# Optimization experiments

Hardware: AMD Instinct MI355X
Metric: run time of the kernel (lower is better)

## Reference

```python
import jax, jax.numpy as jnp
import numpy as np

C = 256      # in/out channels
PSI = 4
W = C // PSI          # window width = 64
D = W // 2            # stride = 32
HEADS = 2 * PSI - 1   # 7


def conv_bn_relu(x, Wmat, scale, bias):
    # 1x1 conv (no bias) + inference-mode BN (folded to per-channel scale/bias) + ReLU
    y = jnp.einsum('oc,bcn->bon', Wmat, x)
    return jax.nn.relu(y * scale[:, None] + bias[:, None])


def setup_inputs() -> dict:
    key = jax.random.key(0)
    ks = jax.random.split(key, 16)
    B, N = 4, 2048
    x = jax.random.normal(ks[0], (B, C, N), dtype=jnp.float32)
    Wq = jax.random.normal(ks[1], (C, C), dtype=jnp.float32) / np.sqrt(C)
    Wk = jax.random.normal(ks[2], (C, C), dtype=jnp.float32) / np.sqrt(C)
    Wv = jax.random.normal(ks[3], (C, C), dtype=jnp.float32) / np.sqrt(C)
    sq = jax.random.uniform(ks[4], (C,), dtype=jnp.float32, minval=0.5, maxval=1.5)
    bq = jax.random.normal(ks[5], (C,), dtype=jnp.float32) * 0.1
    sk = jax.random.uniform(ks[6], (C,), dtype=jnp.float32, minval=0.5, maxval=1.5)
    bk = jax.random.normal(ks[7], (C,), dtype=jnp.float32) * 0.1
    sv = jax.random.uniform(ks[8], (C,), dtype=jnp.float32, minval=0.5, maxval=1.5)
    bv = jax.random.normal(ks[9], (C,), dtype=jnp.float32) * 0.1
    Wf = jax.random.normal(ks[10], (C, HEADS * W), dtype=jnp.float32) / np.sqrt(HEADS * W)
    bf = jax.random.normal(ks[11], (C,), dtype=jnp.float32) * 0.1
    sf = jax.random.uniform(ks[12], (C,), dtype=jnp.float32, minval=0.5, maxval=1.5)
    bff = jax.random.normal(ks[13], (C,), dtype=jnp.float32) * 0.1
    return dict(x=x, Wq=Wq, sq=sq, bq=bq, Wk=Wk, sk=sk, bk=bk,
                Wv=Wv, sv=sv, bv=bv, Wf=Wf, bf=bf, sf=sf, bff=bff)


def reference(x, Wq, sq, bq, Wk, sk, bk, Wv, sv, bv, Wf, bf, sf, bff):
    q = conv_bn_relu(x, Wq, sq, bq)   # [B, C, N]
    k = conv_bn_relu(x, Wk, sk, bk)
    v = conv_bn_relu(x, Wv, sv, bv)

    # overlapping channel windows: head m covers channels [m*D, m*D+W)
    win = jnp.arange(HEADS)[:, None] * D + jnp.arange(W)[None, :]  # [HEADS, W]
    qw = q[:, win, :]  # [B, HEADS, W, N]
    kw = k[:, win, :]
    vw = v[:, win, :]

    # a_m = q_m^T k_m over channel window -> [B, HEADS, N, N]
    attn = jnp.einsum('bhwn,bhwm->bhnm', qw, kw)
    attn = jax.nn.softmax(attn, axis=-1)
    # o_m = (a_m v_m^T)^T -> [B, HEADS, W, N]
    o = jnp.einsum('bhnm,bhwm->bhwn', attn, vw)

    B, _, _, N = o.shape
    O = o.reshape(B, HEADS * W, N)  # concat heads along channel dim

    # fusion: 1x1 conv (with bias) + BN + ReLU
    y = jnp.einsum('oc,bcn->bon', Wf, O) + bf[:, None]
    return jax.nn.relu(y * sf[:, None] + bff[:, None])
```

## Files before the change

kernel.cpp:

```cpp
#include <hip/hip_runtime.h>
#include <hip/hip_bf16.h>

typedef __attribute__((ext_vector_type(8))) short bf16x8;
typedef __attribute__((ext_vector_type(4))) float f32x4;

namespace {
constexpr int kC = 256;
constexpr int kN = 2048;
constexpr int kB = 4;
constexpr int kHeads = 7;
constexpr int kOC = kHeads * 64;
constexpr int kSplit = 2;
constexpr int kMChunk = kN / kSplit;
constexpr float kLog2e = 1.44269504f;
}

static __device__ __forceinline__ float bf2f(ushort u) {
    union { unsigned u; float f; } v; v.u = ((unsigned)u) << 16;
    return v.f;
}
static __device__ __forceinline__ unsigned pk_bf16(float a, float b) {
    __hip_bfloat162 h = __float22bfloat162_rn(make_float2(a, b));
    union { __hip_bfloat162 h; unsigned u; } v; v.h = h;
    return v.u;
}
static __device__ __forceinline__ ushort4 pack4bf(float a, float b, float c, float d) {
    union { ushort4 s; uint2 u; } v;
    v.u.x = pk_bf16(a, b); v.u.y = pk_bf16(c, d);
    return v.s;
}
static __device__ __forceinline__ float fexp2(float x) {
#if __has_builtin(__builtin_amdgcn_exp2f)
    return __builtin_amdgcn_exp2f(x);
#else
    return exp2f(x);
#endif
}
static __device__ __forceinline__ void g2l16(const ushort* g, ushort* l) {
    __builtin_amdgcn_global_load_lds(
        (const __attribute__((address_space(1))) void*)g,
        (__attribute__((address_space(3))) void*)l,
        16, 0, 0);
}

__global__ __launch_bounds__(256) void cast_w_kernel(
    const float* __restrict__ Wq, const float* __restrict__ Wk,
    const float* __restrict__ Wv, const float* __restrict__ Wf,
    ushort* __restrict__ wq, ushort* __restrict__ wk,
    ushort* __restrict__ wv, ushort* __restrict__ wf)
{
    int which = blockIdx.y;
    const float* src = which == 0 ? Wq : which == 1 ? Wk : which == 2 ? Wv : Wf;
    ushort* dst      = which == 0 ? wq : which == 1 ? wk : which == 2 ? wv : wf;
    int n = (which == 3) ? kC * kOC : kC * kC;
    int i = (blockIdx.x * 256 + threadIdx.x) * 4;
    if (i < n) {
        float4 v = *(const float4*)(src + i);
        *(ushort4*)(dst + i) = pack4bf(v.x, v.y, v.z, v.w);
    }
}

__global__ __launch_bounds__(256) void transpose_kernel(
    const float* __restrict__ x, ushort* __restrict__ xT)
{
    const int nt = blockIdx.x, ct = blockIdx.y, b = blockIdx.z;
    __shared__ float T[64][65];
    const int tid = threadIdx.x;
    const float* xb = x + ((size_t)b * kC + ct * 64) * kN + nt * 64;
#pragma unroll
    for (int p = 0; p < 16; ++p) {
        int idx = p * 256 + tid;
        int cc = idx >> 6, nn = idx & 63;
        T[cc][nn] = xb[(size_t)cc * kN + nn];
    }
    __syncthreads();
    ushort* xTb = xT + ((size_t)b * kN + nt * 64) * kC + ct * 64;
#pragma unroll
    for (int p = 0; p < 4; ++p) {
        int nn = p * 16 + (tid >> 4);
        int c4 = (tid & 15) * 4;
        *(ushort4*)&xTb[(size_t)nn * kC + c4] =
            pack4bf(T[c4 + 0][nn], T[c4 + 1][nn], T[c4 + 2][nn], T[c4 + 3][nn]);
    }
}

__global__ __launch_bounds__(256, 2) void qkv_kernel(
    const ushort* __restrict__ xT,
    const ushort* __restrict__ Wqb, const ushort* __restrict__ Wkb, const ushort* __restrict__ Wvb,
    const float* __restrict__ sq, const float* __restrict__ bq,
    const float* __restrict__ sk, const float* __restrict__ bk,
    const float* __restrict__ sv, const float* __restrict__ bv,
    ushort* __restrict__ qT, ushort* __restrict__ kT, ushort* __restrict__ vB)
{
    const int nt  = blockIdx.x;
    const int ot  = blockIdx.y;
    const int b   = blockIdx.z / 3;
    const int mat = blockIdx.z % 3;
    const ushort* Wb = mat == 0 ? Wqb : mat == 1 ? Wkb : Wvb;
    const float* sm = mat == 0 ? sq : mat == 1 ? sk : sv;
    const float* bm = mat == 0 ? bq : mat == 1 ? bk : bv;

    __shared__ __align__(16) ushort lds[4][128 * 64];

    const int tid = threadIdx.x;
    const int lane = tid & 63, wav = tid >> 6;
    const int quad = lane >> 4, l16 = lane & 15;

    const ushort* xTb = xT + ((size_t)b * kN + nt * 128) * kC;
    const ushort* Wt  = Wb + (size_t)(ot * 128) * kC;

    f32x4 acc[8][2];
#pragma unroll
    for (int mt = 0; mt < 8; ++mt)
#pragma unroll
        for (int ntt = 0; ntt < 2; ++ntt)
#pragma unroll
            for (int r = 0; r < 4; ++r) acc[mt][ntt][r] = 0.f;

    const int sa   = lane >> 3;
    const int sblk = (lane & 7) ^ sa;
    auto dmaK = [&](int k0, int buf) {
#pragma unroll
        for (int p = 0; p < 4; ++p) {
            int row = wav * 32 + p * 8 + sa;
            size_t so = (size_t)row * kC + k0 + sblk * 8;
            int dbase = (wav * 32 + p * 8) * 64;
            g2l16(Wt + so,  &lds[buf][dbase]);
            g2l16(xTb + so, &lds[2 + buf][dbase]);
        }
    };

    dmaK(0, 0);
    __syncthreads();

    for (int kt = 0; kt < 4; ++kt) {
        const int cur = kt & 1;
        const bool more = (kt < 3);
        if (more) dmaK((kt + 1) * 64, cur ^ 1);

        const ushort* rowB = (mat < 2) ? lds[cur] : lds[2 + cur];
        const ushort* colB = (mat < 2) ? lds[2 + cur] : lds[cur];
#pragma unroll
        for (int ks = 0; ks < 2; ++ks) {
            bf16x8 bfr[2];
#pragma unroll
            for (int ntt = 0; ntt < 2; ++ntt) {
                int row = wav * 32 + ntt * 16 + l16;
                bfr[ntt] = *(const bf16x8*)&colB[row * 64 + (((ks * 4 + quad) ^ (row & 7)) * 8)];
            }
#pragma unroll
            for (int mt = 0; mt < 8; ++mt) {
                int row = mt * 16 + l16;
                bf16x8 af = *(const bf16x8*)&rowB[row * 64 + (((ks * 4 + quad) ^ (row & 7)) * 8)];
#pragma unroll
                for (int ntt = 0; ntt < 2; ++ntt)
                    acc[mt][ntt] = __builtin_amdgcn_mfma_f32_16x16x32_bf16(
                        af, bfr[ntt], acc[mt][ntt], 0, 0, 0);
            }
        }
        __syncthreads();
    }

    ushort* sT = &lds[0][0];
    const float qs = (mat == 0) ? kLog2e : 1.f;

    if (mat < 2) {
#pragma unroll
        for (int mt = 0; mt < 8; ++mt) {
            float4 sc4 = *(const float4*)&sm[ot * 128 + mt * 16 + quad * 4];
            float4 bi4 = *(const float4*)&bm[ot * 128 + mt * 16 + quad * 4];
#pragma unroll
            for (int ntt = 0; ntt < 2; ++ntt) {
                int nrow = wav * 32 + ntt * 16 + l16;
                float v0 = fmaf(acc[mt][ntt][0], sc4.x, bi4.x) * qs;
                float v1 = fmaf(acc[mt][ntt][1], sc4.y, bi4.y) * qs;
                float v2 = fmaf(acc[mt][ntt][2], sc4.z, bi4.z) * qs;
                float v3 = fmaf(acc[mt][ntt][3], sc4.w, bi4.w) * qs;
                int cb = (mt * 2 + (quad >> 1)) ^ (nrow & 15);
                *(ushort4*)&sT[nrow * 128 + cb * 8 + (quad & 1) * 4] =
                    pack4bf(v0 > 0.f ? v0 : 0.f, v1 > 0.f ? v1 : 0.f,
                            v2 > 0.f ? v2 : 0.f, v3 > 0.f ? v3 : 0.f);
            }
        }
        __syncthreads();
        ushort* out = (mat == 0) ? qT : kT;
#pragma unroll
        for (int p = 0; p < 8; ++p) {
            int idx = p * 256 + tid;
            int row = idx >> 4, blk = idx & 15;
            int4 d = *(const int4*)&sT[row * 128 + ((blk ^ (row & 15)) * 8)];
            *(int4*)&out[((size_t)b * kN + nt * 128 + row) * kC + ot * 128 + blk * 8] = d;
        }
    } else {
#pragma unroll
        for (int ntt = 0; ntt < 2; ++ntt) {
            int orow = wav * 32 + ntt * 16 + l16;
            float sc = sm[ot * 128 + orow], bi = bm[ot * 128 + orow];
#pragma unroll
            for (int mt = 0; mt < 8; ++mt) {
                float v0 = fmaf(acc[mt][ntt][0], sc, bi);
                float v1 = fmaf(acc[mt][ntt][1], sc, bi);
                float v2 = fmaf(acc[mt][ntt][2], sc, bi);
                float v3 = fmaf(acc[mt][ntt][3], sc, bi);
                int cb = (mt * 2 + (quad >> 1)) ^ (orow & 15);
                *(ushort4*)&sT[orow * 128 + cb * 8 + (quad & 1) * 4] =
                    pack4bf(v0 > 0.f ? v0 : 0.f, v1 > 0.f ? v1 : 0.f,
                            v2 > 0.f ? v2 : 0.f, v3 > 0.f ? v3 : 0.f);
            }
        }
        __syncthreads();
#pragma unroll
        for (int p = 0; p < 8; ++p) {
            int idx = p * 256 + tid;
            int row = idx >> 4, blk = idx & 15;
            int4 d = *(const int4*)&sT[row * 128 + ((blk ^ (row & 15)) * 8)];
            *(int4*)&vB[((size_t)b * kC + ot * 128 + row) * kN + nt * 128 + blk * 8] = d;
        }
    }
}

__global__ __launch_bounds__(512, 4) void attn_kernel(
    const ushort* __restrict__ qT, const ushort* __restrict__ kT,
    const ushort* __restrict__ vB,
    ushort* __restrict__ Opart, float* __restrict__ Ls)
{
    const int j   = blockIdx.x;
    const int lid = (j & 7) * 56 + (j >> 3);
    const int nt  = lid & 7;
    const int rest = lid >> 3;
    const int h = rest % 7;
    const int z = rest / 7;
    const int s = z & 1;
    const int b = z >> 1;
    const int n0 = nt * 256;

    const int tid = threadIdx.x;
    const int lane = tid & 63, wav = tid >> 6;
    const int quad = lane >> 4, l16 = lane & 15;

    __shared__ __align__(16) ushort sKV[2][8192];

    const ushort* qTb = qT + (size_t)b * kN * kC;
    const ushort* kTb = kT + (size_t)b * kN * kC;
    const ushort* vbb = vB + ((size_t)b * kC + h * 32) * kN;

    const int arr   = wav >> 2;
    const int rbase = (wav & 3) * 16;

    bf16x8 qf[2][2];
#pragma unroll
    for (int kk = 0; kk < 2; ++kk)
#pragma unroll
        for (int nt2 = 0; nt2 < 2; ++nt2) {
            int ng = n0 + wav * 32 + nt2 * 16 + l16;
            qf[kk][nt2] = *(const bf16x8*)(qTb + (size_t)ng * kC + h * 32 + kk * 32 + quad * 8);
        }

    f32x4 oacc[4][2];
#pragma unroll
    for (int wt = 0; wt < 4; ++wt)
#pragma unroll
        for (int nt2 = 0; nt2 < 2; ++nt2)
#pragma unroll
            for (int r = 0; r < 4; ++r) oacc[wt][nt2][r] = 0.f;
    float li[2] = {0.f, 0.f};

    const int mstart = s * kMChunk;
    const int NIT = kMChunk / 64;

    const int sa   = lane >> 3;
    const int sblk = (lane & 7) ^ sa;
    auto dmaTile = [&](int m0, int buf) {
#pragma unroll
        for (int p = 0; p < 2; ++p) {
            int rl = rbase + p * 8 + sa;
            const ushort* src = (arr == 0)
                ? (kTb + (size_t)(m0 + rl) * kC + h * 32 + sblk * 8)
                : (vbb + (size_t)rl * kN + m0 + sblk * 8);
            g2l16(src, &sKV[buf][arr * 4096 + (rbase + p * 8) * 64]);
        }
    };

    dmaTile(mstart, 0);
    __syncthreads();

    for (int it = 0; it < NIT; ++it) {
        const int cur = it & 1;
        const bool more = (it + 1 < NIT);
        if (more) dmaTile(mstart + (it + 1) * 64, cur ^ 1);

        const ushort* sK = &sKV[cur][0];
        const ushort* sV = &sKV[cur][4096];

        f32x4 sacc[4][2];
#pragma unroll
        for (int mt = 0; mt < 4; ++mt)
#pragma unroll
            for (int nt2 = 0; nt2 < 2; ++nt2)
#pragma unroll
                for (int r = 0; r < 4; ++r) sacc[mt][nt2][r] = 0.f;
        __builtin_amdgcn_s_setprio(1);
#pragma unroll
        for (int kk = 0; kk < 2; ++kk)
#pragma unroll
            for (int mt = 0; mt < 4; ++mt) {
                int row = mt * 16 + l16;
                bf16x8 af = *(const bf16x8*)&sK[row * 64 + (((kk * 4 + quad) ^ (row & 7)) * 8)];
#pragma unroll
                for (int nt2 = 0; nt2 < 2; ++nt2)
                    sacc[mt][nt2] = __builtin_amdgcn_mfma_f32_16x16x32_bf16(
                        af, qf[kk][nt2], sacc[mt][nt2], 0, 0, 0);
            }
        __builtin_amdgcn_s_setprio(0);

        unsigned d[2][4][2];
#pragma unroll
        for (int nt2 = 0; nt2 < 2; ++nt2) {
            float sum = 0.f;
#pragma unroll
            for (int mt = 0; mt < 4; ++mt) {
                float p0 = fexp2(sacc[mt][nt2][0]);
                float p1 = fexp2(sacc[mt][nt2][1]);
                float p2 = fexp2(sacc[mt][nt2][2]);
                float p3 = fexp2(sacc[mt][nt2][3]);
                sum += (p0 + p1) + (p2 + p3);
                d[nt2][mt][0] = pk_bf16(p0, p1);
                d[nt2][mt][1] = pk_bf16(p2, p3);
            }
            sum += __shfl_xor(sum, 16);
            sum += __shfl_xor(sum, 32);
            li[nt2] += sum;
        }

#pragma unroll
        for (int ks = 0; ks < 2; ++ks) {
            bf16x8 pf[2];
#pragma unroll
            for (int nt2 = 0; nt2 < 2; ++nt2) {
                union { unsigned w[4]; bf16x8 v8; } pu;
#if __has_builtin(__builtin_amdgcn_permlane32_swap) && __has_builtin(__builtin_amdgcn_permlane16_swap)
#pragma unroll
                for (int rd = 0; rd < 2; ++rd) {
                    unsigned a = d[nt2][2 * ks][rd], bb = d[nt2][2 * ks + 1][rd];
                    auto r32 = __builtin_amdgcn_permlane32_swap(a, bb, false, false);
                    auto r16 = __builtin_amdgcn_permlane16_swap(r32[0], r32[1], false, false);
                    pu.w[rd]     = r16[0];
                    pu.w[2 + rd] = r16[1];
                }
#else
                const int gx = ((lane & 16) << 1) + l16;
                const int gy = gx + 16;
                const bool lo = (lane < 32);
#pragma unroll
                for (int rd = 0; rd < 2; ++rd) {
                    unsigned u = d[nt2][2 * ks][rd], v = d[nt2][2 * ks + 1][rd];
                    unsigned xu = (unsigned)__shfl((int)u, gx);
                    unsigned xv = (unsigned)__shfl((int)v, gx);
                    unsigned yu = (unsigned)__shfl((int)u, gy);
                    unsigned yv = (unsigned)__shfl((int)v, gy);
                    pu.w[rd]     = lo ? xu : xv;
                    pu.w[2 + rd] = lo ? yu : yv;
                }
#endif
                pf[nt2] = pu.v8;
            }
            __builtin_amdgcn_s_setprio(1);
#pragma unroll
            for (int wt = 0; wt < 4; ++wt) {
                int wr = wt * 16 + l16;
                bf16x8 vf = *(const bf16x8*)&sV[wr * 64 + (((ks * 4 + quad) ^ (wr & 7)) * 8)];
#pragma unroll
                for (int nt2 = 0; nt2 < 2; ++nt2)
                    oacc[wt][nt2] = __builtin_amdgcn_mfma_f32_16x16x32_bf16(
                        vf, pf[nt2], oacc[wt][nt2], 0, 0, 0);
            }
            __builtin_amdgcn_s_setprio(0);
        }

        __syncthreads();
    }

#pragma unroll
    for (int nt2 = 0; nt2 < 2; ++nt2) {
        if (quad == 0) {
            int n = n0 + wav * 32 + nt2 * 16 + l16;
            size_t si = ((size_t)(s * kB + b) * kHeads + h) * kN + n;
            Ls[si] = li[nt2];
        }
    }
    ushort* sT = &sKV[0][0];
#pragma unroll
    for (int wt = 0; wt < 4; ++wt)
#pragma unroll
        for (int nt2 = 0; nt2 < 2; ++nt2) {
            float inv = 1.f / li[nt2];
            int nrow = wav * 32 + nt2 * 16 + l16;
            int cb = (wt * 2 + (quad >> 1)) ^ (nrow & 7);
            *(ushort4*)&sT[nrow * 64 + cb * 8 + (quad & 1) * 4] =
                pack4bf(oacc[wt][nt2][0] * inv, oacc[wt][nt2][1] * inv,
                        oacc[wt][nt2][2] * inv, oacc[wt][nt2][3] * inv);
        }
    __syncthreads();
    int rsub = tid >> 3, blk = tid & 7;
#pragma unroll
    for (int p = 0; p < 4; ++p) {
        int row = p * 64 + rsub;
        int4 dd = *(const int4*)&sT[row * 64 + ((blk ^ (row & 7)) * 8)];
        *(int4*)&Opart[((size_t)s * kB * kN + (size_t)b * kN + n0 + row) * kOC
                       + h * 64 + blk * 8] = dd;
    }
}

__global__ __launch_bounds__(256, 4) void proj_kernel(
    const ushort* __restrict__ Opart, const float* __restrict__ Ls,
    const ushort* __restrict__ Wfb,
    const float* __restrict__ bf_, const float* __restrict__ sf,
    const float* __restrict__ bff, float* __restrict__ out)
{
    const int nt = blockIdx.x;
    const int ot = blockIdx.y;
    const int b  = blockIdx.z;
    __shared__ __align__(16) ushort sA[2][64 * 64];
    __shared__ __align__(16) ushort sB[2][64 * 64];
    const int tid = threadIdx.x;
    const int lane = tid & 63, wav = tid >> 6;
    const int quad = lane >> 4, l16 = lane & 15;

    const ushort* Wt  = Wfb + (size_t)(ot * 64) * kOC;
    const ushort* Op1 = Opart;
    const ushort* Op2 = Opart + (size_t)kB * kN * kOC;
    const size_t soff = (size_t)kB * kHeads * kN;

    f32x4 acc[4];
#pragma unroll
    for (int ntt = 0; ntt < 4; ++ntt)
#pragma unroll
        for (int r = 0; r < 4; ++r) acc[ntt][r] = 0.f;

    int4 areg[2], b1reg[2], b2reg[2];
    float w1a[2], w2a[2];

    auto prefetch = [&](int kt) {
        int k0 = kt * 64;
#pragma unroll
        for (int p = 0; p < 2; ++p) {
            int idx = p * 256 + tid, row = idx >> 3, blk = idx & 7;
            areg[p] = *(const int4*)(Wt + (size_t)row * kOC + k0 + blk * 8);
            int n = nt * 64 + row;
            size_t bo = ((size_t)b * kN + n) * kOC + k0 + blk * 8;
            b1reg[p] = *(const int4*)(Op1 + bo);
            b2reg[p] = *(const int4*)(Op2 + bo);
            size_t si = ((size_t)b * kHeads + kt) * kN + n;
            float l1 = Ls[si], l2 = Ls[si + soff];
            float inv = 1.f / (l1 + l2);
            w1a[p] = l1 * inv; w2a[p] = l2 * inv;
        }
    };
    auto stage = [&](int buf) {
#pragma unroll
        for (int p = 0; p < 2; ++p) {
            int idx = p * 256 + tid, row = idx >> 3, blk = idx & 7;
            *(int4*)&sA[buf][row * 64 + ((blk ^ (row & 7)) * 8)] = areg[p];
            union { int4 v; ushort u[8]; } a, c;
            a.v = b1reg[p]; c.v = b2reg[p];
            float rr[8];
#pragma unroll
            for (int j = 0; j < 8; ++j)
                rr[j] = bf2f(a.u[j]) * w1a[p] + bf2f(c.u[j]) * w2a[p];
            int4 o;
            o.x = (int)pk_bf16(rr[0], rr[1]);
            o.y = (int)pk_bf16(rr[2], rr[3]);
            o.z = (int)pk_bf16(rr[4], rr[5]);
            o.w = (int)pk_bf16(rr[6], rr[7]);
            *(int4*)&sB[buf][row * 64 + ((blk ^ (row & 7)) * 8)] = o;
        }
    };

    prefetch(0);
    stage(0);
    __syncthreads();

    for (int kt = 0; kt < 7; ++kt) {
        const int cur = kt & 1;
        const bool more = (kt < 6);
        if (more) prefetch(kt + 1);
#pragma unroll
        for (int ks = 0; ks < 2; ++ks) {
            int arow = wav * 16 + l16;
            bf16x8 af = *(const bf16x8*)&sA[cur][arow * 64 + (((ks * 4 + quad) ^ (arow & 7)) * 8)];
#pragma unroll
            for (int ntt = 0; ntt < 4; ++ntt) {
                int brow = ntt * 16 + l16;
                bf16x8 bfr = *(const bf16x8*)&sB[cur][brow * 64 + (((ks * 4 + quad) ^ (brow & 7)) * 8)];
                acc[ntt] = __builtin_amdgcn_mfma_f32_16x16x32_bf16(af, bfr, acc[ntt], 0, 0, 0);
            }
        }
        if (more) stage(cur ^ 1);
        __syncthreads();
    }
#pragma unroll
    for (int r = 0; r < 4; ++r) {
        int o = ot * 64 + wav * 16 + quad * 4 + r;
        float bfv = bf_[o], sfv = sf[o], bffv = bff[o];
#pragma unroll
        for (int ntt = 0; ntt < 4; ++ntt) {
            int n = nt * 64 + ntt * 16 + l16;
            float y = fmaf(acc[ntt][r] + bfv, sfv, bffv);
            out[((size_t)b * kC + o) * kN + n] = y > 0.f ? y : 0.f;
        }
    }
}

extern "C" void kernel_launch(void* const* d_in, const int* in_sizes, int n_in,
                              void* d_out, int out_size, void* d_ws, size_t ws_size,
                              hipStream_t stream) {
    const float* x   = (const float*)d_in[0];
    const float* Wq  = (const float*)d_in[1];
    const float* sq  = (const float*)d_in[2];
    const float* bq  = (const float*)d_in[3];
    const float* Wk  = (const float*)d_in[4];
    const float* sk  = (const float*)d_in[5];
    const float* bk  = (const float*)d_in[6];
    const float* Wv  = (const float*)d_in[7];
    const float* sv  = (const float*)d_in[8];
    const float* bv  = (const float*)d_in[9];
    const float* Wf  = (const float*)d_in[10];
    const float* bf_ = (const float*)d_in[11];
    const float* sf  = (const float*)d_in[12];
    const float* bff = (const float*)d_in[13];
    float* out = (float*)d_out;

    char* ws = (char*)d_ws;
    ushort* xT  = (ushort*)(ws);
    ushort* Wqb = (ushort*)(ws + 4194304);
    ushort* Wkb = (ushort*)(ws + 4325376);
    ushort* Wvb = (ushort*)(ws + 4456448);
    ushort* Wfb = (ushort*)(ws + 4587520);
    ushort* qT  = (ushort*)(ws + 4816896);
    ushort* kT  = (ushort*)(ws + 9011200);
    ushort* vB  = (ushort*)(ws + 13205504);
    ushort* Opart = (ushort*)(ws + 17399808);
    float*  Ls  = (float*)(ws + 32079872);

    cast_w_kernel<<<dim3(112, 4), 256, 0, stream>>>(Wq, Wk, Wv, Wf, Wqb, Wkb, Wvb, Wfb);
    transpose_kernel<<<dim3(kN / 64, kC / 64, kB), 256, 0, stream>>>(x, xT);
    qkv_kernel<<<dim3(kN / 128, kC / 128, kB * 3), 256, 0, stream>>>(
        xT, Wqb, Wkb, Wvb, sq, bq, sk, bk, sv, bv, qT, kT, vB);
    attn_kernel<<<dim3(448), 512, 0, stream>>>(
        qT, kT, vB, Opart, Ls);
    proj_kernel<<<dim3(kN / 64, kC / 64, kB), 256, 0, stream>>>(
        Opart, Ls, Wfb, bf_, sf, bff, out);
}
```

Measured before the change: 156.7 us.

## Double attention KV tile to 128 keys and fuse weight cast with transpose

The attention kernel now stages 128 key/value columns per iteration instead of 64, processing them in two halves. This halves the number of barrier-synchronized iterations and defers the row-sum shuffle reduction to once per tile. The V tile layout is widened to 128 columns with a 16-way XOR swizzle, and the LDS buffer doubles to 64 KB, which may reduce occupancy. Separately, the weight-cast and input-transpose kernels are merged into one launch to save a kernel launch.

```diff
diff --git a/kernel.cpp b/kernel.cpp
--- a/kernel.cpp
+++ b/kernel.cpp
@@ -43,44 +43,46 @@
         16, 0, 0);
 }
 
-__global__ __launch_bounds__(256) void cast_w_kernel(
+__global__ __launch_bounds__(256) void prep_kernel(
+    const float* __restrict__ x,
     const float* __restrict__ Wq, const float* __restrict__ Wk,
     const float* __restrict__ Wv, const float* __restrict__ Wf,
+    ushort* __restrict__ xT,
     ushort* __restrict__ wq, ushort* __restrict__ wk,
     ushort* __restrict__ wv, ushort* __restrict__ wf)
 {
-    int which = blockIdx.y;
-    const float* src = which == 0 ? Wq : which == 1 ? Wk : which == 2 ? Wv : Wf;
-    ushort* dst      = which == 0 ? wq : which == 1 ? wk : which == 2 ? wv : wf;
-    int n = (which == 3) ? kC * kOC : kC * kC;
-    int i = (blockIdx.x * 256 + threadIdx.x) * 4;
-    if (i < n) {
-        float4 v = *(const float4*)(src + i);
-        *(ushort4*)(dst + i) = pack4bf(v.x, v.y, v.z, v.w);
-    }
-}
-
-__global__ __launch_bounds__(256) void transpose_kernel(
-    const float* __restrict__ x, ushort* __restrict__ xT)
-{
-    const int nt = blockIdx.x, ct = blockIdx.y, b = blockIdx.z;
     __shared__ float T[64][65];
+    const int bid = blockIdx.x;
     const int tid = threadIdx.x;
-    const float* xb = x + ((size_t)b * kC + ct * 64) * kN + nt * 64;
-#pragma unroll
-    for (int p = 0; p < 16; ++p) {
-        int idx = p * 256 + tid;
-        int cc = idx >> 6, nn = idx & 63;
-        T[cc][nn] = xb[(size_t)cc * kN + nn];
-    }
-    __syncthreads();
-    ushort* xTb = xT + ((size_t)b * kN + nt * 64) * kC + ct * 64;
-#pragma unroll
-    for (int p = 0; p < 4; ++p) {
-        int nn = p * 16 + (tid >> 4);
-        int c4 = (tid & 15) * 4;
-        *(ushort4*)&xTb[(size_t)nn * kC + c4] =
-            pack4bf(T[c4 + 0][nn], T[c4 + 1][nn], T[c4 + 2][nn], T[c4 + 3][nn]);
+    if (bid < 512) {
+        const int nt = bid & 31, ct = (bid >> 5) & 3, b = bid >> 7;
+        const float* xb = x + ((size_t)b * kC + ct * 64) * kN + nt * 64;
+#pragma unroll
+        for (int p = 0; p < 16; ++p) {
+            int idx = p * 256 + tid;
+            int cc = idx >> 6, nn = idx & 63;
+            T[cc][nn] = xb[(size_t)cc * kN + nn];
+        }
+        __syncthreads();
+        ushort* xTb = xT + ((size_t)b * kN + nt * 64) * kC + ct * 64;
+#pragma unroll
+        for (int p = 0; p < 4; ++p) {
+            int nn = p * 16 + (tid >> 4);
+            int c4 = (tid & 15) * 4;
+            *(ushort4*)&xTb[(size_t)nn * kC + c4] =
+                pack4bf(T[c4 + 0][nn], T[c4 + 1][nn], T[c4 + 2][nn], T[c4 + 3][nn]);
+        }
+    } else {
+        const int j = bid - 512;
+        const int which = j / 112, bx = j % 112;
+        const float* src = which == 0 ? Wq : which == 1 ? Wk : which == 2 ? Wv : Wf;
+        ushort* dst      = which == 0 ? wq : which == 1 ? wk : which == 2 ? wv : wf;
+        int n = (which == 3) ? kC * kOC : kC * kC;
+        int i = (bx * 256 + tid) * 4;
+        if (i < n) {
+            float4 v = *(const float4*)(src + i);
+            *(ushort4*)(dst + i) = pack4bf(v.x, v.y, v.z, v.w);
+        }
     }
 }
 
@@ -238,14 +240,13 @@
     const int lane = tid & 63, wav = tid >> 6;
     const int quad = lane >> 4, l16 = lane & 15;
 
-    __shared__ __align__(16) ushort sKV[2][8192];
+    __shared__ __align__(16) ushort sKV[2][16384];
 
     const ushort* qTb = qT + (size_t)b * kN * kC;
     const ushort* kTb = kT + (size_t)b * kN * kC;
     const ushort* vbb = vB + ((size_t)b * kC + h * 32) * kN;
 
-    const int arr   = wav >> 2;
-    const int rbase = (wav & 3) * 16;
+    const int arr = wav >> 2;
 
     bf16x8 qf[2][2];
 #pragma unroll
@@ -266,18 +267,26 @@
     float li[2] = {0.f, 0.f};
 
     const int mstart = s * kMChunk;
-    const int NIT = kMChunk / 64;
+    const int NIT = kMChunk / 128;
 
     const int sa   = lane >> 3;
     const int sblk = (lane & 7) ^ sa;
     auto dmaTile = [&](int m0, int buf) {
-#pragma unroll
-        for (int p = 0; p < 2; ++p) {
-            int rl = rbase + p * 8 + sa;
-            const ushort* src = (arr == 0)
-                ? (kTb + (size_t)(m0 + rl) * kC + h * 32 + sblk * 8)
-                : (vbb + (size_t)rl * kN + m0 + sblk * 8);
-            g2l16(src, &sKV[buf][arr * 4096 + (rbase + p * 8) * 64]);
+        if (arr == 0) {
+#pragma unroll
+            for (int p = 0; p < 4; ++p) {
+                int rl = (wav & 3) * 32 + p * 8 + sa;
+                g2l16(kTb + (size_t)(m0 + rl) * kC + h * 32 + sblk * 8,
+                      &sKV[buf][((wav & 3) * 32 + p * 8) * 64]);
+            }
+        } else {
+#pragma unroll
+            for (int p = 0; p < 4; ++p) {
+                int rw = (wav & 3) * 16 + p * 4 + (lane >> 4);
+                int vb = (lane & 15) ^ (rw & 15);
+                g2l16(vbb + (size_t)rw * kN + m0 + vb * 8,
+                      &sKV[buf][8192 + ((wav & 3) * 16 + p * 4) * 128]);
+            }
         }
     };
 
@@ -287,95 +296,107 @@
     for (int it = 0; it < NIT; ++it) {
         const int cur = it & 1;
         const bool more = (it + 1 < NIT);
-        if (more) dmaTile(mstart + (it + 1) * 64, cur ^ 1);
+        if (more) dmaTile(mstart + (it + 1) * 128, cur ^ 1);
 
         const ushort* sK = &sKV[cur][0];
-        const ushort* sV = &sKV[cur][4096];
-
-        f32x4 sacc[4][2];
-#pragma unroll
-        for (int mt = 0; mt < 4; ++mt)
-#pragma unroll
-            for (int nt2 = 0; nt2 < 2; ++nt2)
-#pragma unroll
-                for (int r = 0; r < 4; ++r) sacc[mt][nt2][r] = 0.f;
-        __builtin_amdgcn_s_setprio(1);
-#pragma unroll
-        for (int kk = 0; kk < 2; ++kk)
-#pragma unroll
-            for (int mt = 0; mt < 4; ++mt) {
-                int row = mt * 16 + l16;
-                bf16x8 af = *(const bf16x8*)&sK[row * 64 + (((kk * 4 + quad) ^ (row & 7)) * 8)];
+        const ushort* sV = &sKV[cur][8192];
+
+        float rs0 = 0.f, rs1 = 0.f;
+
+#pragma unroll
+        for (int half = 0; half < 2; ++half) {
+            f32x4 sacc[4][2];
+#pragma unroll
+            for (int mt = 0; mt < 4; ++mt)
 #pragma unroll
                 for (int nt2 = 0; nt2 < 2; ++nt2)
-                    sacc[mt][nt2] = __builtin_amdgcn_mfma_f32_16x16x32_bf16(
-                        af, qf[kk][nt2], sacc[mt][nt2], 0, 0, 0);
-            }
-        __builtin_amdgcn_s_setprio(0);
-
-        unsigned d[2][4][2];
-#pragma unroll
-        for (int nt2 = 0; nt2 < 2; ++nt2) {
-            float sum = 0.f;
-#pragma unroll
-            for (int mt = 0; mt < 4; ++mt) {
-                float p0 = fexp2(sacc[mt][nt2][0]);
-                float p1 = fexp2(sacc[mt][nt2][1]);
-                float p2 = fexp2(sacc[mt][nt2][2]);
-                float p3 = fexp2(sacc[mt][nt2][3]);
-                sum += (p0 + p1) + (p2 + p3);
-                d[nt2][mt][0] = pk_bf16(p0, p1);
-                d[nt2][mt][1] = pk_bf16(p2, p3);
-            }
-            sum += __shfl_xor(sum, 16);
-            sum += __shfl_xor(sum, 32);
-            li[nt2] += sum;
-        }
-
-#pragma unroll
-        for (int ks = 0; ks < 2; ++ks) {
-            bf16x8 pf[2];
-#pragma unroll
-            for (int nt2 = 0; nt2 < 2; ++nt2) {
-                union { unsigned w[4]; bf16x8 v8; } pu;
+#pragma unroll
+                    for (int r = 0; r < 4; ++r) sacc[mt][nt2][r] = 0.f;
+            __builtin_amdgcn_s_setprio(1);
+#pragma unroll
+            for (int kk = 0; kk < 2; ++kk)
+#pragma unroll
+                for (int mt = 0; mt < 4; ++mt) {
+                    int row = half * 64 + mt * 16 + l16;
+                    bf16x8 af = *(const bf16x8*)&sK[row * 64 + (((kk * 4 + quad) ^ (row & 7)) * 8)];
+#pragma unroll
+                    for (int nt2 = 0; nt2 < 2; ++nt2)
+                        sacc[mt][nt2] = __builtin_amdgcn_mfma_f32_16x16x32_bf16(
+                            af, qf[kk][nt2], sacc[mt][nt2], 0, 0, 0);
+                }
+            __builtin_amdgcn_s_setprio(0);
+
+#pragma unroll
+            for (int ksp = 0; ksp < 2; ++ksp) {
+                const int G = half * 2 + ksp;
+                unsigned d[2][2][2];
+#pragma unroll
+                for (int nt2 = 0; nt2 < 2; ++nt2) {
+                    float sum = 0.f;
+#pragma unroll
+                    for (int mi = 0; mi < 2; ++mi) {
+                        int mt = 2 * ksp + mi;
+                        float p0 = fexp2(sacc[mt][nt2][0]);
+                        float p1 = fexp2(sacc[mt][nt2][1]);
+                        float p2 = fexp2(sacc[mt][nt2][2]);
+                        float p3 = fexp2(sacc[mt][nt2][3]);
+                        sum += (p0 + p1) + (p2 + p3);
+                        d[nt2][mi][0] = pk_bf16(p0, p1);
+                        d[nt2][mi][1] = pk_bf16(p2, p3);
+                    }
+                    if (nt2 == 0) rs0 += sum; else rs1 += sum;
+                }
+
+                bf16x8 pf[2];
+#pragma unroll
+                for (int nt2 = 0; nt2 < 2; ++nt2) {
+                    union { unsigned w[4]; bf16x8 v8; } pu;
 #if __has_builtin(__builtin_amdgcn_permlane32_swap) && __has_builtin(__builtin_amdgcn_permlane16_swap)
 #pragma unroll
-                for (int rd = 0; rd < 2; ++rd) {
-                    unsigned a = d[nt2][2 * ks][rd], bb = d[nt2][2 * ks + 1][rd];
-                    auto r32 = __builtin_amdgcn_permlane32_swap(a, bb, false, false);
-                    auto r16 = __builtin_amdgcn_permlane16_swap(r32[0], r32[1], false, false);
-                    pu.w[rd]     = r16[0];
-                    pu.w[2 + rd] = r16[1];
+                    for (int rd = 0; rd < 2; ++rd) {
+                        unsigned a = d[nt2][0][rd], bb = d[nt2][1][rd];
+                        auto r32 = __builtin_amdgcn_permlane32_swap(a, bb, false, false);
+                        auto r16 = __builtin_amdgcn_permlane16_swap(r32[0], r32[1], false, false);
+                        pu.w[rd]     = r16[0];
+                        pu.w[2 + rd] = r16[1];
+                    }
+#else
+                    const int gx = ((lane & 16) << 1) + l16;
+                    const int gy = gx + 16;
+                    const bool lo = (lane < 32);
+#pragma unroll
+                    for (int rd = 0; rd < 2; ++rd) {
+                        unsigned u = d[nt2][0][rd], v = d[nt2][1][rd];
+                        unsigned xu = (unsigned)__shfl((int)u, gx);
+                        unsigned xv = (unsigned)__shfl((int)v, gx);
+                        unsigned yu = (unsigned)__shfl((int)u, gy);
+                        unsigned yv = (unsigned)__shfl((int)v, gy);
+                        pu.w[rd]     = lo ? xu : xv;
+                        pu.w[2 + rd] = lo ? yu : yv;
+                    }
+#endif
+                    pf[nt2] = pu.v8;
                 }
-#else
-                const int gx = ((lane & 16) << 1) + l16;
-                const int gy = gx + 16;
-                const bool lo = (lane < 32);
-#pragma unroll
-                for (int rd = 0; rd < 2; ++rd) {
-                    unsigned u = d[nt2][2 * ks][rd], v = d[nt2][2 * ks + 1][rd];
-                    unsigned xu = (unsigned)__shfl((int)u, gx);
-                    unsigned xv = (unsigned)__shfl((int)v, gx);
-                    unsigned yu = (unsigned)__shfl((int)u, gy);
-                    unsigned yv = (unsigned)__shfl((int)v, gy);
-                    pu.w[rd]     = lo ? xu : xv;
-                    pu.w[2 + rd] = lo ? yu : yv;
+                __builtin_amdgcn_s_setprio(1);
+#pragma unroll
+                for (int wt = 0; wt < 4; ++wt) {
+                    int wr = wt * 16 + l16;
+                    bf16x8 vf = *(const bf16x8*)&sV[wr * 128 + (((G * 4 + quad) ^ (wr & 15)) * 8)];
+#pragma unroll
+                    for (int nt2 = 0; nt2 < 2; ++nt2)
+                        oacc[wt][nt2] = __builtin_amdgcn_mfma_f32_16x16x32_bf16(
+                            vf, pf[nt2], oacc[wt][nt2], 0, 0, 0);
                 }
-#endif
-                pf[nt2] = pu.v8;
-            }
-            __builtin_amdgcn_s_setprio(1);
-#pragma unroll
-            for (int wt = 0; wt < 4; ++wt) {
-                int wr = wt * 16 + l16;
-                bf16x8 vf = *(const bf16x8*)&sV[wr * 64 + (((ks * 4 + quad) ^ (wr & 7)) * 8)];
-#pragma unroll
-                for (int nt2 = 0; nt2 < 2; ++nt2)
-                    oacc[wt][nt2] = __builtin_amdgcn_mfma_f32_16x16x32_bf16(
-                        vf, pf[nt2], oacc[wt][nt2], 0, 0, 0);
-            }
-            __builtin_amdgcn_s_setprio(0);
-        }
+                __builtin_amdgcn_s_setprio(0);
+            }
+        }
+
+        rs0 += __shfl_xor(rs0, 16);
+        rs0 += __shfl_xor(rs0, 32);
+        rs1 += __shfl_xor(rs1, 16);
+        rs1 += __shfl_xor(rs1, 32);
+        li[0] += rs0;
+        li[1] += rs1;
 
         __syncthreads();
     }
@@ -465,8 +486,8 @@
             a.v = b1reg[p]; c.v = b2reg[p];
             float rr[8];
 #pragma unroll
-            for (int j = 0; j < 8; ++j)
-                rr[j] = bf2f(a.u[j]) * w1a[p] + bf2f(c.u[j]) * w2a[p];
+            for (int jj = 0; jj < 8; ++jj)
+                rr[jj] = bf2f(a.u[jj]) * w1a[p] + bf2f(c.u[jj]) * w2a[p];
             int4 o;
             o.x = (int)pk_bf16(rr[0], rr[1]);
             o.y = (int)pk_bf16(rr[2], rr[3]);
@@ -542,8 +563,8 @@
     ushort* Opart = (ushort*)(ws + 17399808);
     float*  Ls  = (float*)(ws + 32079872);
 
-    cast_w_kernel<<<dim3(112, 4), 256, 0, stream>>>(Wq, Wk, Wv, Wf, Wqb, Wkb, Wvb, Wfb);
-    transpose_kernel<<<dim3(kN / 64, kC / 64, kB), 256, 0, stream>>>(x, xT);
+    prep_kernel<<<dim3(960), 256, 0, stream>>>(
+        x, Wq, Wk, Wv, Wf, xT, Wqb, Wkb, Wvb, Wfb);
     qkv_kernel<<<dim3(kN / 128, kC / 128, kB * 3), 256, 0, stream>>>(
         xT, Wqb, Wkb, Wvb, sq, bq, sk, bk, sv, bv, qT, kT, vB);
     attn_kernel<<<dim3(448), 512, 0, stream>>>(
```

New measurement: 194.3 us. 1.24x slower.

## Triple-buffer attention K/V tiles with partial vmcnt waits and merge prep kernels

Applied to the files above, without the earlier changes.

The attention kernel moves from double to triple buffering of K/V tiles in LDS. It prefetches two tiles ahead and uses explicit s_waitcnt vmcnt(2) barriers, so only the oldest tile's DMA has to complete before each step. Launch bounds drop to 2 blocks per CU to make room for the extra LDS buffer. Separately, the weight-cast and input-transpose kernels are merged into one launch to save launch overhead. The lower occupancy could offset the gain from deeper prefetch.

```diff
diff --git a/kernel.cpp b/kernel.cpp
--- a/kernel.cpp
+++ b/kernel.cpp
@@ -42,45 +42,59 @@
         (__attribute__((address_space(3))) void*)l,
         16, 0, 0);
 }
-
-__global__ __launch_bounds__(256) void cast_w_kernel(
+static __device__ __forceinline__ void tile_barrier2() {
+    __builtin_amdgcn_sched_barrier(0);
+    asm volatile("s_waitcnt vmcnt(2)" ::: "memory");
+    __builtin_amdgcn_s_barrier();
+    __builtin_amdgcn_sched_barrier(0);
+}
+static __device__ __forceinline__ void tile_barrier0() {
+    __builtin_amdgcn_sched_barrier(0);
+    asm volatile("s_waitcnt vmcnt(0)" ::: "memory");
+    __builtin_amdgcn_s_barrier();
+    __builtin_amdgcn_sched_barrier(0);
+}
+
+__global__ __launch_bounds__(256) void prep_kernel(
+    const float* __restrict__ x,
     const float* __restrict__ Wq, const float* __restrict__ Wk,
     const float* __restrict__ Wv, const float* __restrict__ Wf,
+    ushort* __restrict__ xT,
     ushort* __restrict__ wq, ushort* __restrict__ wk,
     ushort* __restrict__ wv, ushort* __restrict__ wf)
 {
-    int which = blockIdx.y;
-    const float* src = which == 0 ? Wq : which == 1 ? Wk : which == 2 ? Wv : Wf;
-    ushort* dst      = which == 0 ? wq : which == 1 ? wk : which == 2 ? wv : wf;
-    int n = (which == 3) ? kC * kOC : kC * kC;
-    int i = (blockIdx.x * 256 + threadIdx.x) * 4;
-    if (i < n) {
-        float4 v = *(const float4*)(src + i);
-        *(ushort4*)(dst + i) = pack4bf(v.x, v.y, v.z, v.w);
-    }
-}
-
-__global__ __launch_bounds__(256) void transpose_kernel(
-    const float* __restrict__ x, ushort* __restrict__ xT)
-{
-    const int nt = blockIdx.x, ct = blockIdx.y, b = blockIdx.z;
     __shared__ float T[64][65];
+    const int bid = blockIdx.x;
     const int tid = threadIdx.x;
-    const float* xb = x + ((size_t)b * kC + ct * 64) * kN + nt * 64;
-#pragma unroll
-    for (int p = 0; p < 16; ++p) {
-        int idx = p * 256 + tid;
-        int cc = idx >> 6, nn = idx & 63;
-        T[cc][nn] = xb[(size_t)cc * kN + nn];
-    }
-    __syncthreads();
-    ushort* xTb = xT + ((size_t)b * kN + nt * 64) * kC + ct * 64;
-#pragma unroll
-    for (int p = 0; p < 4; ++p) {
-        int nn = p * 16 + (tid >> 4);
-        int c4 = (tid & 15) * 4;
-        *(ushort4*)&xTb[(size_t)nn * kC + c4] =
-            pack4bf(T[c4 + 0][nn], T[c4 + 1][nn], T[c4 + 2][nn], T[c4 + 3][nn]);
+    if (bid < 512) {
+        const int nt = bid & 31, ct = (bid >> 5) & 3, b = bid >> 7;
+        const float* xb = x + ((size_t)b * kC + ct * 64) * kN + nt * 64;
+#pragma unroll
+        for (int p = 0; p < 16; ++p) {
+            int idx = p * 256 + tid;
+            int cc = idx >> 6, nn = idx & 63;
+            T[cc][nn] = xb[(size_t)cc * kN + nn];
+        }
+        __syncthreads();
+        ushort* xTb = xT + ((size_t)b * kN + nt * 64) * kC + ct * 64;
+#pragma unroll
+        for (int p = 0; p < 4; ++p) {
+            int nn = p * 16 + (tid >> 4);
+            int c4 = (tid & 15) * 4;
+            *(ushort4*)&xTb[(size_t)nn * kC + c4] =
+                pack4bf(T[c4 + 0][nn], T[c4 + 1][nn], T[c4 + 2][nn], T[c4 + 3][nn]);
+        }
+    } else {
+        const int j = bid - 512;
+        const int which = j / 112, bx = j % 112;
+        const float* src = which == 0 ? Wq : which == 1 ? Wk : which == 2 ? Wv : Wf;
+        ushort* dst      = which == 0 ? wq : which == 1 ? wk : which == 2 ? wv : wf;
+        int n = (which == 3) ? kC * kOC : kC * kC;
+        int i = (bx * 256 + tid) * 4;
+        if (i < n) {
+            float4 v = *(const float4*)(src + i);
+            *(ushort4*)(dst + i) = pack4bf(v.x, v.y, v.z, v.w);
+        }
     }
 }
 
@@ -219,7 +233,7 @@
     }
 }
 
-__global__ __launch_bounds__(512, 4) void attn_kernel(
+__global__ __launch_bounds__(512, 2) void attn_kernel(
     const ushort* __restrict__ qT, const ushort* __restrict__ kT,
     const ushort* __restrict__ vB,
     ushort* __restrict__ Opart, float* __restrict__ Ls)
@@ -238,7 +252,7 @@
     const int lane = tid & 63, wav = tid >> 6;
     const int quad = lane >> 4, l16 = lane & 15;
 
-    __shared__ __align__(16) ushort sKV[2][8192];
+    __shared__ __align__(16) ushort sKV[3][8192];
 
     const ushort* qTb = qT + (size_t)b * kN * kC;
     const ushort* kTb = kT + (size_t)b * kN * kC;
@@ -282,12 +296,16 @@
     };
 
     dmaTile(mstart, 0);
-    __syncthreads();
-
+    dmaTile(mstart + 64, 1);
+    tile_barrier2();
+
+    int cur = 0;
     for (int it = 0; it < NIT; ++it) {
-        const int cur = it & 1;
-        const bool more = (it + 1 < NIT);
-        if (more) dmaTile(mstart + (it + 1) * 64, cur ^ 1);
+        const bool deep = (it + 2 < NIT);
+        if (deep) {
+            int fut = cur + 2; if (fut >= 3) fut -= 3;
+            dmaTile(mstart + (it + 2) * 64, fut);
+        }
 
         const ushort* sK = &sKV[cur][0];
         const ushort* sV = &sKV[cur][4096];
@@ -377,7 +395,9 @@
             __builtin_amdgcn_s_setprio(0);
         }
 
-        __syncthreads();
+        if (deep) tile_barrier2();
+        else      tile_barrier0();
+        cur = (cur == 2) ? 0 : cur + 1;
     }
 
 #pragma unroll
@@ -465,8 +485,8 @@
             a.v = b1reg[p]; c.v = b2reg[p];
             float rr[8];
 #pragma unroll
-            for (int j = 0; j < 8; ++j)
-                rr[j] = bf2f(a.u[j]) * w1a[p] + bf2f(c.u[j]) * w2a[p];
+            for (int jj = 0; jj < 8; ++jj)
+                rr[jj] = bf2f(a.u[jj]) * w1a[p] + bf2f(c.u[jj]) * w2a[p];
             int4 o;
             o.x = (int)pk_bf16(rr[0], rr[1]);
             o.y = (int)pk_bf16(rr[2], rr[3]);
@@ -542,8 +562,8 @@
     ushort* Opart = (ushort*)(ws + 17399808);
     float*  Ls  = (float*)(ws + 32079872);
 
-    cast_w_kernel<<<dim3(112, 4), 256, 0, stream>>>(Wq, Wk, Wv, Wf, Wqb, Wkb, Wvb, Wfb);
-    transpose_kernel<<<dim3(kN / 64, kC / 64, kB), 256, 0, stream>>>(x, xT);
+    prep_kernel<<<dim3(960), 256, 0, stream>>>(
+        x, Wq, Wk, Wv, Wf, xT, Wqb, Wkb, Wvb, Wfb);
     qkv_kernel<<<dim3(kN / 128, kC / 128, kB * 3), 256, 0, stream>>>(
         xT, Wqb, Wkb, Wvb, sq, bq, sk, bk, sv, bv, qT, kT, vB);
     attn_kernel<<<dim3(448), 512, 0, stream>>>(
```

Measured after the change: 151.7 us. 1.03x faster.

## Drop attention key split, fuse prep kernels, stream proj operands via LDS DMA

Applied to the files above, without the earlier changes.

Removes the two-way split over keys in the attention kernel, so each block covers all 2048 keys. This eliminates the partial-sum buffer Ls and the weighted recombination step in the projection kernel. The projection kernel now loads its W and O tiles directly into LDS with global_load_lds DMA instead of going through registers, and reads only one Opart. The row-sum shuffle reduction is moved out of the inner loop, and the weight-cast and transpose kernels are merged into one launch. The cost is that attention now launches 224 blocks, each twice as long, which may underfill the GPU.

```diff
diff --git a/kernel.cpp b/kernel.cpp
--- a/kernel.cpp
+++ b/kernel.cpp
@@ -10,8 +10,6 @@
 constexpr int kB = 4;
 constexpr int kHeads = 7;
 constexpr int kOC = kHeads * 64;
-constexpr int kSplit = 2;
-constexpr int kMChunk = kN / kSplit;
 constexpr float kLog2e = 1.44269504f;
 }
 
@@ -43,44 +41,46 @@
         16, 0, 0);
 }
 
-__global__ __launch_bounds__(256) void cast_w_kernel(
+__global__ __launch_bounds__(256) void prep_kernel(
+    const float* __restrict__ x,
     const float* __restrict__ Wq, const float* __restrict__ Wk,
     const float* __restrict__ Wv, const float* __restrict__ Wf,
+    ushort* __restrict__ xT,
     ushort* __restrict__ wq, ushort* __restrict__ wk,
     ushort* __restrict__ wv, ushort* __restrict__ wf)
 {
-    int which = blockIdx.y;
-    const float* src = which == 0 ? Wq : which == 1 ? Wk : which == 2 ? Wv : Wf;
-    ushort* dst      = which == 0 ? wq : which == 1 ? wk : which == 2 ? wv : wf;
-    int n = (which == 3) ? kC * kOC : kC * kC;
-    int i = (blockIdx.x * 256 + threadIdx.x) * 4;
-    if (i < n) {
-        float4 v = *(const float4*)(src + i);
-        *(ushort4*)(dst + i) = pack4bf(v.x, v.y, v.z, v.w);
-    }
-}
-
-__global__ __launch_bounds__(256) void transpose_kernel(
-    const float* __restrict__ x, ushort* __restrict__ xT)
-{
-    const int nt = blockIdx.x, ct = blockIdx.y, b = blockIdx.z;
     __shared__ float T[64][65];
+    const int bid = blockIdx.x;
     const int tid = threadIdx.x;
-    const float* xb = x + ((size_t)b * kC + ct * 64) * kN + nt * 64;
-#pragma unroll
-    for (int p = 0; p < 16; ++p) {
-        int idx = p * 256 + tid;
-        int cc = idx >> 6, nn = idx & 63;
-        T[cc][nn] = xb[(size_t)cc * kN + nn];
-    }
-    __syncthreads();
-    ushort* xTb = xT + ((size_t)b * kN + nt * 64) * kC + ct * 64;
-#pragma unroll
-    for (int p = 0; p < 4; ++p) {
-        int nn = p * 16 + (tid >> 4);
-        int c4 = (tid & 15) * 4;
-        *(ushort4*)&xTb[(size_t)nn * kC + c4] =
-            pack4bf(T[c4 + 0][nn], T[c4 + 1][nn], T[c4 + 2][nn], T[c4 + 3][nn]);
+    if (bid < 512) {
+        const int nt = bid & 31, ct = (bid >> 5) & 3, b = bid >> 7;
+        const float* xb = x + ((size_t)b * kC + ct * 64) * kN + nt * 64;
+#pragma unroll
+        for (int p = 0; p < 16; ++p) {
+            int idx = p * 256 + tid;
+            int cc = idx >> 6, nn = idx & 63;
+            T[cc][nn] = xb[(size_t)cc * kN + nn];
+        }
+        __syncthreads();
+        ushort* xTb = xT + ((size_t)b * kN + nt * 64) * kC + ct * 64;
+#pragma unroll
+        for (int p = 0; p < 4; ++p) {
+            int nn = p * 16 + (tid >> 4);
+            int c4 = (tid & 15) * 4;
+            *(ushort4*)&xTb[(size_t)nn * kC + c4] =
+                pack4bf(T[c4 + 0][nn], T[c4 + 1][nn], T[c4 + 2][nn], T[c4 + 3][nn]);
+        }
+    } else {
+        const int j = bid - 512;
+        const int which = j / 112, bx = j % 112;
+        const float* src = which == 0 ? Wq : which == 1 ? Wk : which == 2 ? Wv : Wf;
+        ushort* dst      = which == 0 ? wq : which == 1 ? wk : which == 2 ? wv : wf;
+        int n = (which == 3) ? kC * kOC : kC * kC;
+        int i = (bx * 256 + tid) * 4;
+        if (i < n) {
+            float4 v = *(const float4*)(src + i);
+            *(ushort4*)(dst + i) = pack4bf(v.x, v.y, v.z, v.w);
+        }
     }
 }
 
@@ -219,20 +219,18 @@
     }
 }
 
-__global__ __launch_bounds__(512, 4) void attn_kernel(
+__global__ __launch_bounds__(512, 2) void attn_kernel(
     const ushort* __restrict__ qT, const ushort* __restrict__ kT,
     const ushort* __restrict__ vB,
-    ushort* __restrict__ Opart, float* __restrict__ Ls)
+    ushort* __restrict__ Opart)
 {
     const int j   = blockIdx.x;
-    const int lid = (j & 7) * 56 + (j >> 3);
-    const int nt  = lid & 7;
-    const int rest = lid >> 3;
-    const int h = rest % 7;
-    const int z = rest / 7;
-    const int s = z & 1;
-    const int b = z >> 1;
-    const int n0 = nt * 256;
+    const int lid = (j & 7) * 28 + (j >> 3);
+    const int b   = lid / 56;
+    const int r2  = lid % 56;
+    const int h   = r2 % 7;
+    const int nt  = r2 / 7;
+    const int n0  = nt * 256;
 
     const int tid = threadIdx.x;
     const int lane = tid & 63, wav = tid >> 6;
@@ -265,8 +263,7 @@
             for (int r = 0; r < 4; ++r) oacc[wt][nt2][r] = 0.f;
     float li[2] = {0.f, 0.f};
 
-    const int mstart = s * kMChunk;
-    const int NIT = kMChunk / 64;
+    const int NIT = kN / 64;
 
     const int sa   = lane >> 3;
     const int sblk = (lane & 7) ^ sa;
@@ -281,13 +278,13 @@
         }
     };
 
-    dmaTile(mstart, 0);
+    dmaTile(0, 0);
     __syncthreads();
 
     for (int it = 0; it < NIT; ++it) {
         const int cur = it & 1;
         const bool more = (it + 1 < NIT);
-        if (more) dmaTile(mstart + (it + 1) * 64, cur ^ 1);
+        if (more) dmaTile((it + 1) * 64, cur ^ 1);
 
         const ushort* sK = &sKV[cur][0];
         const ushort* sV = &sKV[cur][4096];
@@ -327,8 +324,6 @@
                 d[nt2][mt][0] = pk_bf16(p0, p1);
                 d[nt2][mt][1] = pk_bf16(p2, p3);
             }
-            sum += __shfl_xor(sum, 16);
-            sum += __shfl_xor(sum, 32);
             li[nt2] += sum;
         }
 
@@ -382,11 +377,8 @@
 
 #pragma unroll
     for (int nt2 = 0; nt2 < 2; ++nt2) {
-        if (quad == 0) {
-            int n = n0 + wav * 32 + nt2 * 16 + l16;
-            size_t si = ((size_t)(s * kB + b) * kHeads + h) * kN + n;
-            Ls[si] = li[nt2];
-        }
+        li[nt2] += __shfl_xor(li[nt2], 16);
+        li[nt2] += __shfl_xor(li[nt2], 32);
     }
     ushort* sT = &sKV[0][0];
 #pragma unroll
@@ -406,14 +398,12 @@
     for (int p = 0; p < 4; ++p) {
         int row = p * 64 + rsub;
         int4 dd = *(const int4*)&sT[row * 64 + ((blk ^ (row & 7)) * 8)];
-        *(int4*)&Opart[((size_t)s * kB * kN + (size_t)b * kN + n0 + row) * kOC
-                       + h * 64 + blk * 8] = dd;
+        *(int4*)&Opart[((size_t)b * kN + n0 + row) * kOC + h * 64 + blk * 8] = dd;
     }
 }
 
 __global__ __launch_bounds__(256, 4) void proj_kernel(
-    const ushort* __restrict__ Opart, const float* __restrict__ Ls,
-    const ushort* __restrict__ Wfb,
+    const ushort* __restrict__ Opart, const ushort* __restrict__ Wfb,
     const float* __restrict__ bf_, const float* __restrict__ sf,
     const float* __restrict__ bff, float* __restrict__ out)
 {
@@ -426,10 +416,8 @@
     const int lane = tid & 63, wav = tid >> 6;
     const int quad = lane >> 4, l16 = lane & 15;
 
-    const ushort* Wt  = Wfb + (size_t)(ot * 64) * kOC;
-    const ushort* Op1 = Opart;
-    const ushort* Op2 = Opart + (size_t)kB * kN * kOC;
-    const size_t soff = (size_t)kB * kHeads * kN;
+    const ushort* Wt = Wfb + (size_t)(ot * 64) * kOC;
+    const ushort* Ob = Opart + ((size_t)b * kN + nt * 64) * kOC;
 
     f32x4 acc[4];
 #pragma unroll
@@ -437,53 +425,26 @@
 #pragma unroll
         for (int r = 0; r < 4; ++r) acc[ntt][r] = 0.f;
 
-    int4 areg[2], b1reg[2], b2reg[2];
-    float w1a[2], w2a[2];
-
-    auto prefetch = [&](int kt) {
+    const int sa   = lane >> 3;
+    const int sblk = (lane & 7) ^ sa;
+    auto dmaT = [&](int kt, int buf) {
         int k0 = kt * 64;
 #pragma unroll
         for (int p = 0; p < 2; ++p) {
-            int idx = p * 256 + tid, row = idx >> 3, blk = idx & 7;
-            areg[p] = *(const int4*)(Wt + (size_t)row * kOC + k0 + blk * 8);
-            int n = nt * 64 + row;
-            size_t bo = ((size_t)b * kN + n) * kOC + k0 + blk * 8;
-            b1reg[p] = *(const int4*)(Op1 + bo);
-            b2reg[p] = *(const int4*)(Op2 + bo);
-            size_t si = ((size_t)b * kHeads + kt) * kN + n;
-            float l1 = Ls[si], l2 = Ls[si + soff];
-            float inv = 1.f / (l1 + l2);
-            w1a[p] = l1 * inv; w2a[p] = l2 * inv;
+            int row = wav * 16 + p * 8 + sa;
+            int dbase = (wav * 16 + p * 8) * 64;
+            g2l16(Wt + (size_t)row * kOC + k0 + sblk * 8, &sA[buf][dbase]);
+            g2l16(Ob + (size_t)row * kOC + k0 + sblk * 8, &sB[buf][dbase]);
         }
     };
-    auto stage = [&](int buf) {
-#pragma unroll
-        for (int p = 0; p < 2; ++p) {
-            int idx = p * 256 + tid, row = idx >> 3, blk = idx & 7;
-            *(int4*)&sA[buf][row * 64 + ((blk ^ (row & 7)) * 8)] = areg[p];
-            union { int4 v; ushort u[8]; } a, c;
-            a.v = b1reg[p]; c.v = b2reg[p];
-            float rr[8];
-#pragma unroll
-            for (int j = 0; j < 8; ++j)
-                rr[j] = bf2f(a.u[j]) * w1a[p] + bf2f(c.u[j]) * w2a[p];
-            int4 o;
-            o.x = (int)pk_bf16(rr[0], rr[1]);
-            o.y = (int)pk_bf16(rr[2], rr[3]);
-            o.z = (int)pk_bf16(rr[4], rr[5]);
-            o.w = (int)pk_bf16(rr[6], rr[7]);
-            *(int4*)&sB[buf][row * 64 + ((blk ^ (row & 7)) * 8)] = o;
-        }
-    };
-
-    prefetch(0);
-    stage(0);
+
+    dmaT(0, 0);
     __syncthreads();
 
     for (int kt = 0; kt < 7; ++kt) {
         const int cur = kt & 1;
         const bool more = (kt < 6);
-        if (more) prefetch(kt + 1);
+        if (more) dmaT(kt + 1, cur ^ 1);
 #pragma unroll
         for (int ks = 0; ks < 2; ++ks) {
             int arow = wav * 16 + l16;
@@ -495,7 +456,6 @@
                 acc[ntt] = __builtin_amdgcn_mfma_f32_16x16x32_bf16(af, bfr, acc[ntt], 0, 0, 0);
             }
         }
-        if (more) stage(cur ^ 1);
         __syncthreads();
     }
 #pragma unroll
@@ -540,14 +500,13 @@
     ushort* kT  = (ushort*)(ws + 9011200);
     ushort* vB  = (ushort*)(ws + 13205504);
     ushort* Opart = (ushort*)(ws + 17399808);
-    float*  Ls  = (float*)(ws + 32079872);
-
-    cast_w_kernel<<<dim3(112, 4), 256, 0, stream>>>(Wq, Wk, Wv, Wf, Wqb, Wkb, Wvb, Wfb);
-    transpose_kernel<<<dim3(kN / 64, kC / 64, kB), 256, 0, stream>>>(x, xT);
+
+    prep_kernel<<<dim3(960), 256, 0, stream>>>(
+        x, Wq, Wk, Wv, Wf, xT, Wqb, Wkb, Wvb, Wfb);
     qkv_kernel<<<dim3(kN / 128, kC / 128, kB * 3), 256, 0, stream>>>(
         xT, Wqb, Wkb, Wvb, sq, bq, sk, bk, sv, bv, qT, kT, vB);
-    attn_kernel<<<dim3(448), 512, 0, stream>>>(
-        qT, kT, vB, Opart, Ls);
+    attn_kernel<<<dim3(224), 512, 0, stream>>>(
+        qT, kT, vB, Opart);
     proj_kernel<<<dim3(kN / 64, kC / 64, kB), 256, 0, stream>>>(
-        Opart, Ls, Wfb, bf_, sf, bff, out);
-}
+        Opart, Wfb, bf_, sf, bff, out);
+}
```

Result: faster. 153.2 us (-2.2%).
